# Performance work log

Hardware: AMD Instinct MI355X
Metric: run time of the kernel (lower is better)

## Reference

```python
import jax, jax.numpy as jnp
import numpy as np

N_SPK = 2048   # number of speakers
U = 32         # utterances per speaker (half enrollment, half test)
D = 256        # embedding dim
EPS = 1e-8     # F.cosine_similarity eps (norm clamp)


def setup_inputs() -> dict:
    key = jax.random.key(0)
    k1, = jax.random.split(key, 1)
    embeddings = jax.random.normal(k1, (N_SPK * U, D), dtype=jnp.float32)
    labels = jnp.repeat(jnp.arange(N_SPK, dtype=jnp.int64), U)
    alpha = jnp.float32(10.0)
    beta = jnp.float32(-5.0)
    return {"embeddings": embeddings, "labels": labels, "alpha": alpha, "beta": beta}


def _ge2e_loss(embeddings, labels_np, alpha, beta):
    # labels_np: host numpy int labels (constant). Balanced: each speaker has U utts.
    n_spk = int(labels_np.max()) + 1
    u = labels_np.shape[0] // n_spk
    order = np.argsort(labels_np, kind="stable")  # group by speaker, preserve order
    emb = embeddings[order].reshape(n_spk, u, -1)           # [N, U, D]
    half = u // 2
    enroll, test = emb[:, :half], emb[:, half:]             # [N, U/2, D]
    cent = enroll.mean(axis=1)                              # [N, D]
    tn = test / jnp.maximum(jnp.linalg.norm(test, axis=-1, keepdims=True), EPS)
    cn = cent / jnp.maximum(jnp.linalg.norm(cent, axis=-1, keepdims=True), EPS)
    # cosine sim of every test utt (speaker m, utt t) vs every centroid n
    sims = alpha * jnp.einsum("mtd,nd->mtn", tn, cn) + beta  # [N, U/2, N]
    e = jnp.exp(sims)
    total = e.sum(axis=(0, 1))                               # [N] sum over all test utts per centroid
    idx = jnp.arange(n_spk)
    pos_sum = e[idx, :, idx].sum(axis=1)                     # [N] own-speaker test utts
    neg_sum = total - pos_sum                                # sum over other speakers' test utts
    loss = jnp.mean(jnp.log(neg_sum) - jnp.log(pos_sum))
    return loss


def reference(embeddings, labels, alpha, beta):
    labels_np = np.asarray(labels)
    return _ge2e_loss(embeddings, labels_np, alpha, beta)
```

## Files before the change

### kernel.cpp

```cpp
#include <hip/hip_runtime.h>
#include <hip/hip_bf16.h>
#include <stdint.h>

#define N_SPK 2048
#define UU 32
#define DD 256
#define HALF_U 16
#define M_ROWS (N_SPK * HALF_U)

#define BM 256
#define BN 256
#define BK 64

typedef __attribute__((ext_vector_type(8))) short short8;
typedef __attribute__((ext_vector_type(4))) float f32x4;

typedef const __attribute__((address_space(1))) void ga_void;
typedef __attribute__((address_space(3))) void ls_void;

__device__ __forceinline__ void gld16(const void* g, void* l) {
    __builtin_amdgcn_global_load_lds((ga_void*)(uintptr_t)g,
                                     (ls_void*)(uintptr_t)l, 16, 0, 0);
}

__device__ __forceinline__ unsigned short f2bf(float x) {
    union { float f; unsigned u; } c; c.f = x;
    unsigned r = c.u + 0x7fffu + ((c.u >> 16) & 1u);
    return (unsigned short)(r >> 16);
}

__global__ __launch_bounds__(256) void prep_kernel(const float* __restrict__ emb,
                                                   unsigned short* __restrict__ tn,
                                                   unsigned short* __restrict__ cn)
{
    const int w = threadIdx.x >> 6;
    const int l = threadIdx.x & 63;
    const int task = blockIdx.x * 4 + w;

    float4 v;
    if (task < M_ROWS) {
        const int m = task >> 4;
        const int t = task & 15;
        const size_t grow = (size_t)m * UU + HALF_U + t;
        v = *(const float4*)(emb + grow * DD + 4 * l);
    } else {
        const int n = task - M_ROWS;
        float ax = 0.f, ay = 0.f, az = 0.f, aw = 0.f;
        const float* base = emb + (size_t)n * UU * DD + 4 * l;
        #pragma unroll
        for (int j = 0; j < HALF_U; ++j) {
            float4 e = *(const float4*)(base + j * DD);
            ax += e.x; ay += e.y; az += e.z; aw += e.w;
        }
        const float inv = 1.0f / 16.0f;
        v = make_float4(ax * inv, ay * inv, az * inv, aw * inv);
    }
    float ss = v.x * v.x + v.y * v.y + v.z * v.z + v.w * v.w;
    #pragma unroll
    for (int d = 1; d < 64; d <<= 1) ss += __shfl_xor(ss, d);
    const float sc = 1.0f / fmaxf(sqrtf(ss), 1e-8f);

    ushort4 o;
    o.x = f2bf(v.x * sc); o.y = f2bf(v.y * sc);
    o.z = f2bf(v.z * sc); o.w = f2bf(v.w * sc);
    unsigned short* dst = (task < M_ROWS)
        ? (tn + (size_t)task * DD + 4 * l)
        : (cn + (size_t)(task - M_ROWS) * DD + 4 * l);
    *(ushort4*)dst = o;
}

__device__ __forceinline__ void stage_kt(const char* gA, const char* gB,
                                         char* lA, char* lB, int ktb, int tid)
{
    #pragma unroll
    for (int i = 0; i < 4; ++i) {
        const int off = i * 8192 + tid * 16;
        const int row = off >> 7;
        const int sc  = ((off >> 4) & 7) ^ (row & 7);
        const int goff = row * 512 + ktb + sc * 16;
        gld16(gA + goff, lA + off);
        gld16(gB + goff, lB + off);
    }
}

__device__ __forceinline__ void compute_kt(const char* Asb, const char* Bsb,
                                           f32x4 (&acc)[8][4],
                                           int wr, int wc, int r16, int hi)
{
    #pragma unroll
    for (int kk = 0; kk < 2; ++kk) {
        short8 b[4];
        #pragma unroll
        for (int ni = 0; ni < 4; ++ni) {
            const int row = wc * 64 + ni * 16 + r16;
            const int c16 = (kk * 4 + hi) ^ (row & 7);
            b[ni] = *(const short8*)(Bsb + row * 128 + c16 * 16);
        }
        #pragma unroll
        for (int mi = 0; mi < 8; ++mi) {
            const int row = wr * 128 + mi * 16 + r16;
            const int c16 = (kk * 4 + hi) ^ (row & 7);
            const short8 a = *(const short8*)(Asb + row * 128 + c16 * 16);
            #pragma unroll
            for (int ni = 0; ni < 4; ++ni)
                acc[mi][ni] = __builtin_amdgcn_mfma_f32_16x16x32_bf16(
                    a, b[ni], acc[mi][ni], 0, 0, 0);
        }
    }
}

#define WAITVM(n) do { \
    asm volatile("s_waitcnt vmcnt(" #n ")" ::: "memory"); \
    __builtin_amdgcn_sched_barrier(0); \
} while (0)

__global__ __launch_bounds__(512, 1) void gemm_kernel(const unsigned short* __restrict__ tnb,
                                                      const unsigned short* __restrict__ cnb,
                                                      const float* __restrict__ alphaP,
                                                      const float* __restrict__ betaP,
                                                      float* __restrict__ total,
                                                      float* __restrict__ pos)
{
    __shared__ __align__(16) char As[2][BM * BK * 2];
    __shared__ __align__(16) char Bs[2][BN * BK * 2];

    const int tid = threadIdx.x;
    const int l = tid & 63;
    const int w = tid >> 6;
    const int wr = w >> 2, wc = w & 3;
    const int r16 = l & 15, hi = l >> 4;

    const int bid = blockIdx.x;
    const int tile = (bid & 7) * 128 + (bid >> 3);
    const int bm = tile >> 3;
    const int bn = tile & 7;

    const char* gA = (const char*)tnb + (size_t)bm * BM * 512;
    const char* gB = (const char*)cnb + (size_t)bn * BN * 512;

    f32x4 acc[8][4] = {};

    stage_kt(gA, gB, As[0], Bs[0], 0 * 128, tid);
    stage_kt(gA, gB, As[1], Bs[1], 1 * 128, tid);
    WAITVM(8);
    __builtin_amdgcn_s_barrier();

    compute_kt(As[0], Bs[0], acc, wr, wc, r16, hi);
    __builtin_amdgcn_s_barrier();
    stage_kt(gA, gB, As[0], Bs[0], 2 * 128, tid);
    WAITVM(8);
    __builtin_amdgcn_s_barrier();

    compute_kt(As[1], Bs[1], acc, wr, wc, r16, hi);
    __builtin_amdgcn_s_barrier();
    stage_kt(gA, gB, As[1], Bs[1], 3 * 128, tid);
    WAITVM(8);
    __builtin_amdgcn_s_barrier();

    compute_kt(As[0], Bs[0], acc, wr, wc, r16, hi);
    WAITVM(0);
    __builtin_amdgcn_s_barrier();

    compute_kt(As[1], Bs[1], acc, wr, wc, r16, hi);

    __builtin_amdgcn_s_barrier();
    float* colsum = (float*)As;
    if (tid < BN) colsum[tid] = 0.0f;
    __builtin_amdgcn_s_barrier();

    const float alpha = *alphaP;
    const float beta  = *betaP;

    #pragma unroll
    for (int ni = 0; ni < 4; ++ni) {
        const int colg = bn * BN + wc * 64 + ni * 16 + r16;
        float csum = 0.f;
        #pragma unroll
        for (int mi = 0; mi < 8; ++mi) {
            const int rowbase = bm * BM + wr * 128 + mi * 16 + hi * 4;
            #pragma unroll
            for (int r = 0; r < 4; ++r) {
                const float e = __expf(alpha * acc[mi][ni][r] + beta);
                csum += e;
                if (((rowbase + r) >> 4) == colg)
                    atomicAdd(pos + colg, e);
            }
        }
        csum += __shfl_xor(csum, 16);
        csum += __shfl_xor(csum, 32);
        if (hi == 0) atomicAdd(&colsum[wc * 64 + ni * 16 + r16], csum);
    }
    __syncthreads();
    if (tid < BN) atomicAdd(total + bn * BN + tid, colsum[tid]);
}

__global__ __launch_bounds__(256) void finalize_kernel(const float* __restrict__ total,
                                                       const float* __restrict__ pos,
                                                       float* __restrict__ out)
{
    const int tid = threadIdx.x;
    float s = 0.f;
    for (int i = tid; i < N_SPK; i += 256) {
        const float p = pos[i];
        const float t = total[i];
        s += logf(t - p) - logf(p);
    }
    #pragma unroll
    for (int d = 1; d < 64; d <<= 1) s += __shfl_xor(s, d);
    __shared__ float wsum[4];
    if ((tid & 63) == 0) wsum[tid >> 6] = s;
    __syncthreads();
    if (tid == 0) out[0] = (wsum[0] + wsum[1] + wsum[2] + wsum[3]) * (1.0f / (float)N_SPK);
}

extern "C" void kernel_launch(void* const* d_in, const int* in_sizes, int n_in,
                              void* d_out, int out_size, void* d_ws, size_t ws_size,
                              hipStream_t stream)
{
    const float* emb    = (const float*)d_in[0];
    const float* alphaP = (const float*)d_in[2];
    const float* betaP  = (const float*)d_in[3];
    float* out = (float*)d_out;

    char* ws = (char*)d_ws;
    unsigned short* tn = (unsigned short*)ws;
    unsigned short* cn = (unsigned short*)(ws + 16777216);
    float* total       = (float*)(ws + 16777216 + 1048576);
    float* pos         = total + N_SPK;

    hipMemsetAsync(total, 0, 2 * N_SPK * sizeof(float), stream);

    hipLaunchKernelGGL(prep_kernel, dim3((M_ROWS + N_SPK) / 4), dim3(256), 0, stream,
                       emb, tn, cn);
    hipLaunchKernelGGL(gemm_kernel, dim3(M_ROWS / BM * (N_SPK / BN)), dim3(512), 0, stream,
                       tn, cn, alphaP, betaP, total, pos);
    hipLaunchKernelGGL(finalize_kernel, dim3(1), dim3(256), 0, stream,
                       total, pos, out);
}
```

Measured before the change: 159.5 us.

## Restructure GEMM K-loop into half-tile ring buffer with interleaved staging

Swaps the two-stage full-tile double buffer for a four-slot ring of half tiles. Global-to-LDS loads for the next K step are issued in smaller units between MFMA phases, with barriers and s_setprio raising MFMA priority. Launch bounds are raised to two blocks per CU, and the accumulator memset is folded into the prep kernel to drop one launch. This adds barriers per K step and register pressure, which risks spills at the higher occupancy target.

```diff
diff --git a/kernel.cpp b/kernel.cpp
--- a/kernel.cpp
+++ b/kernel.cpp
@@ -29,10 +29,26 @@
     return (unsigned short)(r >> 16);
 }
 
+#define WAITVM(n) do { \
+    asm volatile("s_waitcnt vmcnt(" #n ")" ::: "memory"); \
+    __builtin_amdgcn_sched_barrier(0); \
+} while (0)
+
+#define WAITLGKM0 do { \
+    asm volatile("s_waitcnt lgkmcnt(0)" ::: "memory"); \
+    __builtin_amdgcn_sched_barrier(0); \
+} while (0)
+
 __global__ __launch_bounds__(256) void prep_kernel(const float* __restrict__ emb,
                                                    unsigned short* __restrict__ tn,
-                                                   unsigned short* __restrict__ cn)
-{
+                                                   unsigned short* __restrict__ cn,
+                                                   float* __restrict__ zbuf)
+{
+    if (blockIdx.x == 0) {
+        #pragma unroll
+        for (int i = 0; i < 16; ++i) zbuf[threadIdx.x + 256 * i] = 0.0f;
+    }
+
     const int w = threadIdx.x >> 6;
     const int l = threadIdx.x & 63;
     const int task = blockIdx.x * 4 + w;
@@ -69,60 +85,14 @@
     *(ushort4*)dst = o;
 }
 
-__device__ __forceinline__ void stage_kt(const char* gA, const char* gB,
-                                         char* lA, char* lB, int ktb, int tid)
-{
-    #pragma unroll
-    for (int i = 0; i < 4; ++i) {
-        const int off = i * 8192 + tid * 16;
-        const int row = off >> 7;
-        const int sc  = ((off >> 4) & 7) ^ (row & 7);
-        const int goff = row * 512 + ktb + sc * 16;
-        gld16(gA + goff, lA + off);
-        gld16(gB + goff, lB + off);
-    }
-}
-
-__device__ __forceinline__ void compute_kt(const char* Asb, const char* Bsb,
-                                           f32x4 (&acc)[8][4],
-                                           int wr, int wc, int r16, int hi)
-{
-    #pragma unroll
-    for (int kk = 0; kk < 2; ++kk) {
-        short8 b[4];
-        #pragma unroll
-        for (int ni = 0; ni < 4; ++ni) {
-            const int row = wc * 64 + ni * 16 + r16;
-            const int c16 = (kk * 4 + hi) ^ (row & 7);
-            b[ni] = *(const short8*)(Bsb + row * 128 + c16 * 16);
-        }
-        #pragma unroll
-        for (int mi = 0; mi < 8; ++mi) {
-            const int row = wr * 128 + mi * 16 + r16;
-            const int c16 = (kk * 4 + hi) ^ (row & 7);
-            const short8 a = *(const short8*)(Asb + row * 128 + c16 * 16);
-            #pragma unroll
-            for (int ni = 0; ni < 4; ++ni)
-                acc[mi][ni] = __builtin_amdgcn_mfma_f32_16x16x32_bf16(
-                    a, b[ni], acc[mi][ni], 0, 0, 0);
-        }
-    }
-}
-
-#define WAITVM(n) do { \
-    asm volatile("s_waitcnt vmcnt(" #n ")" ::: "memory"); \
-    __builtin_amdgcn_sched_barrier(0); \
-} while (0)
-
-__global__ __launch_bounds__(512, 1) void gemm_kernel(const unsigned short* __restrict__ tnb,
+__global__ __launch_bounds__(512, 2) void gemm_kernel(const unsigned short* __restrict__ tnb,
                                                       const unsigned short* __restrict__ cnb,
                                                       const float* __restrict__ alphaP,
                                                       const float* __restrict__ betaP,
                                                       float* __restrict__ total,
                                                       float* __restrict__ pos)
 {
-    __shared__ __align__(16) char As[2][BM * BK * 2];
-    __shared__ __align__(16) char Bs[2][BN * BK * 2];
+    __shared__ __align__(16) char S[4][32768];
 
     const int tid = threadIdx.x;
     const int l = tid & 63;
@@ -130,6 +100,9 @@
     const int wr = w >> 2, wc = w & 3;
     const int r16 = l & 15, hi = l >> 4;
 
+    const float alpha = *alphaP;
+    const float beta  = *betaP;
+
     const int bid = blockIdx.x;
     const int tile = (bid & 7) * 128 + (bid >> 3);
     const int bm = tile >> 3;
@@ -138,38 +111,85 @@
     const char* gA = (const char*)tnb + (size_t)bm * BM * 512;
     const char* gB = (const char*)cnb + (size_t)bn * BN * 512;
 
+    auto stage_unit = [&](int kt, int u) {
+        const int h = u >> 1;
+        const int mat = u & 1;
+        char* slot = S[(2 * kt + h) & 3] + mat * 16384;
+        const char* g = mat ? gB : gA;
+        #pragma unroll
+        for (int i = 0; i < 2; ++i) {
+            const int off = i * 8192 + tid * 16;
+            const int row = off >> 7;
+            const int sc  = ((off >> 4) & 7) ^ (row & 7);
+            const int goff = (h * 128 + row) * 512 + kt * 128 + sc * 16;
+            gld16(g + goff, slot + off);
+        }
+    };
+
     f32x4 acc[8][4] = {};
 
-    stage_kt(gA, gB, As[0], Bs[0], 0 * 128, tid);
-    stage_kt(gA, gB, As[1], Bs[1], 1 * 128, tid);
+    #pragma unroll
+    for (int u = 0; u < 4; ++u) stage_unit(0, u);
+    #pragma unroll
+    for (int u = 0; u < 4; ++u) stage_unit(1, u);
     WAITVM(8);
     __builtin_amdgcn_s_barrier();
 
-    compute_kt(As[0], Bs[0], acc, wr, wc, r16, hi);
-    __builtin_amdgcn_s_barrier();
-    stage_kt(gA, gB, As[0], Bs[0], 2 * 128, tid);
-    WAITVM(8);
-    __builtin_amdgcn_s_barrier();
-
-    compute_kt(As[1], Bs[1], acc, wr, wc, r16, hi);
-    __builtin_amdgcn_s_barrier();
-    stage_kt(gA, gB, As[1], Bs[1], 3 * 128, tid);
-    WAITVM(8);
-    __builtin_amdgcn_s_barrier();
-
-    compute_kt(As[0], Bs[0], acc, wr, wc, r16, hi);
-    WAITVM(0);
-    __builtin_amdgcn_s_barrier();
-
-    compute_kt(As[1], Bs[1], acc, wr, wc, r16, hi);
-
-    __builtin_amdgcn_s_barrier();
-    float* colsum = (float*)As;
+    #pragma unroll
+    for (int kt = 0; kt < 4; ++kt) {
+        const char* As = S[(2 * kt + wr) & 3];
+        const char* Bs = S[(2 * kt + (wc >> 1)) & 3] + 16384;
+        short8 b[4][2];
+        #pragma unroll
+        for (int p = 0; p < 4; ++p) {
+            short8 a[2][2];
+            if (p == 0) {
+                #pragma unroll
+                for (int ni = 0; ni < 4; ++ni)
+                    #pragma unroll
+                    for (int kk = 0; kk < 2; ++kk) {
+                        const int row = wc * 64 + ni * 16 + r16;
+                        const int c16 = (kk * 4 + hi) ^ (row & 7);
+                        b[ni][kk] = *(const short8*)(Bs + (row & 127) * 128 + c16 * 16);
+                    }
+            }
+            #pragma unroll
+            for (int m2 = 0; m2 < 2; ++m2)
+                #pragma unroll
+                for (int kk = 0; kk < 2; ++kk) {
+                    const int mi = p * 2 + m2;
+                    const int lrow = mi * 16 + r16;
+                    const int c16 = (kk * 4 + hi) ^ (lrow & 7);
+                    a[m2][kk] = *(const short8*)(As + lrow * 128 + c16 * 16);
+                }
+            if (kt == 1 || kt == 2) {
+                if (p == 0) { stage_unit(kt + 1, 0); stage_unit(kt + 1, 1); }
+                if (p == 1) { stage_unit(kt + 1, 2); stage_unit(kt + 1, 3); }
+            }
+            __builtin_amdgcn_s_barrier();
+            WAITLGKM0;
+            __builtin_amdgcn_s_setprio(1);
+            #pragma unroll
+            for (int kk = 0; kk < 2; ++kk)
+                #pragma unroll
+                for (int m2 = 0; m2 < 2; ++m2)
+                    #pragma unroll
+                    for (int ni = 0; ni < 4; ++ni)
+                        acc[p * 2 + m2][ni] = __builtin_amdgcn_mfma_f32_16x16x32_bf16(
+                            a[m2][kk], b[ni][kk], acc[p * 2 + m2][ni], 0, 0, 0);
+            __builtin_amdgcn_s_setprio(0);
+            __builtin_amdgcn_s_barrier();
+        }
+        if (kt < 3) {
+            WAITVM(0);
+            __builtin_amdgcn_s_barrier();
+        }
+    }
+
+    float* colsum = (float*)S;
+    __syncthreads();
     if (tid < BN) colsum[tid] = 0.0f;
-    __builtin_amdgcn_s_barrier();
-
-    const float alpha = *alphaP;
-    const float beta  = *betaP;
+    __syncthreads();
 
     #pragma unroll
     for (int ni = 0; ni < 4; ++ni) {
@@ -228,10 +248,8 @@
     float* total       = (float*)(ws + 16777216 + 1048576);
     float* pos         = total + N_SPK;
 
-    hipMemsetAsync(total, 0, 2 * N_SPK * sizeof(float), stream);
-
     hipLaunchKernelGGL(prep_kernel, dim3((M_ROWS + N_SPK) / 4), dim3(256), 0, stream,
-                       emb, tn, cn);
+                       emb, tn, cn, total );
     hipLaunchKernelGGL(gemm_kernel, dim3(M_ROWS / BM * (N_SPK / BN)), dim3(512), 0, stream,
                        tn, cn, alphaP, betaP, total, pos);
     hipLaunchKernelGGL(finalize_kernel, dim3(1), dim3(256), 0, stream,
```

Result: no change. 157.8 us (-1.1%).
